# Kernel tuning notes

Hardware: AMD Instinct MI355X
Metric: run time of the kernel (lower is better)

The kernel has to match this reference:

```python
import jax, jax.numpy as jnp
import numpy as np
import math

D_MODEL = 1024
N_HEADS = 16
D_FF = 4096
KERNEL = 25
EPS = 1e-5


def setup_inputs() -> dict:
    key = jax.random.key(0)
    ks = jax.random.split(key, 16)
    B, L, D = 2, 2048, D_MODEL
    s = 0.02
    inp = {
        'x': jax.random.normal(ks[0], (B, L, D), dtype=jnp.float32),
        'Wq': jax.random.normal(ks[1], (D, D), dtype=jnp.float32) * s,
        'bq': jnp.zeros((D,), jnp.float32),
        'Wk': jax.random.normal(ks[2], (D, D), dtype=jnp.float32) * s,
        'bk': jnp.zeros((D,), jnp.float32),
        'Wv': jax.random.normal(ks[3], (D, D), dtype=jnp.float32) * s,
        'bv': jnp.zeros((D,), jnp.float32),
        'Wo': jax.random.normal(ks[4], (D, D), dtype=jnp.float32) * s,
        'bo': jnp.zeros((D,), jnp.float32),
        'W1': jax.random.normal(ks[5], (D_FF, D), dtype=jnp.float32) * s,
        'b1': jnp.zeros((D_FF,), jnp.float32),
        'W2': jax.random.normal(ks[6], (D, D_FF), dtype=jnp.float32) * s,
        'b2': jnp.zeros((D,), jnp.float32),
        'g1': jnp.ones((D,), jnp.float32),
        'be1': jnp.zeros((D,), jnp.float32),
        'g2': jnp.ones((D,), jnp.float32),
        'be2': jnp.zeros((D,), jnp.float32),
    }
    return inp


def moving_avg(x):
    # torch AvgPool1d(kernel=25, stride=1, padding=12, count_include_pad=True)
    # x: (B, L, D) -> trend: (B, L, D)
    pad = KERNEL // 2
    xp = jnp.pad(x, ((0, 0), (pad, pad), (0, 0)))
    c = jnp.cumsum(xp, axis=1)
    c = jnp.concatenate([jnp.zeros_like(c[:, :1]), c], axis=1)
    return (c[:, KERNEL:] - c[:, :-KERNEL]) / KERNEL


def layernorm(x, g, b):
    mu = jnp.mean(x, axis=-1, keepdims=True)
    var = jnp.mean((x - mu) ** 2, axis=-1, keepdims=True)
    return (x - mu) * jax.lax.rsqrt(var + EPS) * g + b


def reference(x, Wq, bq, Wk, bk, Wv, bv, Wo, bo, W1, b1, W2, b2, g1, be1, g2, be2):
    B, L, D = x.shape
    H, dk = N_HEADS, D // N_HEADS
    # projections (torch Linear: y = x @ W.T + b)
    q = (x @ Wq.T + bq).reshape(B, L, H, dk).transpose(0, 2, 1, 3)
    k = (x @ Wk.T + bk).reshape(B, L, H, dk).transpose(0, 2, 1, 3)
    v = (x @ Wv.T + bv).reshape(B, L, H, dk).transpose(0, 2, 1, 3)
    scores = jnp.einsum('bhld,bhmd->bhlm', q, k) / math.sqrt(dk)
    t = jnp.arange(L, dtype=jnp.float32)
    time_bias = -0.1 * jnp.abs(t[None, :] - t[:, None])  # (L, L)
    attn = jax.nn.softmax(scores + time_bias[None, None], axis=-1)
    ao = jnp.einsum('bhlm,bhmd->bhld', attn, v)
    ao = ao.transpose(0, 2, 1, 3).reshape(B, L, D)
    attn_out = ao @ Wo.T + bo
    x = x + attn_out
    x = moving_avg(x)  # trend kept (x, _ = decomp1(x))
    x = layernorm(x, g1, be1)
    ff = jax.nn.gelu(x @ W1.T + b1, approximate=False) @ W2.T + b2
    x = x + ff
    x = moving_avg(x)  # trend kept again
    x = layernorm(x, g2, be2)
    return x
```

## Files before the change

kernel.cpp:

```cpp
#include <hip/hip_runtime.h>
#include <hip/hip_bf16.h>
#include <math.h>

#define DMODEL 1024
#define LSEQ   2048
#define BATCH  2
#define NHEADS 16
#define DHEAD  64
#define DFF    4096
#define MROWS  (BATCH*LSEQ)

typedef __attribute__((ext_vector_type(8))) short short8;
typedef __attribute__((ext_vector_type(4))) float f32x4;
using bf16 = __hip_bfloat16;

static __device__ __forceinline__ f32x4 mfma16(short8 a, short8 b, f32x4 c) {
    return __builtin_amdgcn_mfma_f32_16x16x32_bf16(a, b, c, 0, 0, 0);
}

static __device__ __forceinline__ void gload16(const void* g, void* l) {
    __builtin_amdgcn_global_load_lds(
        (const __attribute__((address_space(1))) char*)g,
        (__attribute__((address_space(3))) char*)l, 16, 0, 0);
}

static __device__ __forceinline__ bf16 b16(float v) { return __float2bfloat16(v); }

__global__ void f2b1_kernel(const float* __restrict__ in, bf16* __restrict__ out, int n4) {
    int i = blockIdx.x * blockDim.x + threadIdx.x;
    if (i >= n4) return;
    float4 v = reinterpret_cast<const float4*>(in)[i];
    union { ushort4 u; bf16 h[4]; } o;
    o.h[0] = b16(v.x); o.h[1] = b16(v.y); o.h[2] = b16(v.z); o.h[3] = b16(v.w);
    reinterpret_cast<ushort4*>(out)[i] = o.u;
}

__global__ void f2b4_kernel(const float* p0, const float* p1, const float* p2, const float* p3,
                            bf16* o0, bf16* o1, bf16* o2, bf16* o3, int n4) {
    const float* in; bf16* out;
    switch (blockIdx.y) {
        case 0: in = p0; out = o0; break;
        case 1: in = p1; out = o1; break;
        case 2: in = p2; out = o2; break;
        default: in = p3; out = o3; break;
    }
    int i = blockIdx.x * blockDim.x + threadIdx.x;
    if (i >= n4) return;
    float4 v = reinterpret_cast<const float4*>(in)[i];
    union { ushort4 u; bf16 h[4]; } o;
    o.h[0] = b16(v.x); o.h[1] = b16(v.y); o.h[2] = b16(v.z); o.h[3] = b16(v.w);
    reinterpret_cast<ushort4*>(out)[i] = o.u;
}

__global__ void concat3_kernel(const float* __restrict__ a, const float* __restrict__ b,
                               const float* __restrict__ c, float* __restrict__ o) {
    int i = blockIdx.x * blockDim.x + threadIdx.x;
    if (i < DMODEL) { o[i] = a[i]; o[DMODEL + i] = b[i]; o[2 * DMODEL + i] = c[i]; }
}

template<int S>
__global__ __launch_bounds__(256) void reduce_kernel(const float* __restrict__ res,
                                                     const float* __restrict__ P,
                                                     const float* __restrict__ bias,
                                                     float* __restrict__ out, int n4) {
    int i = blockIdx.x * blockDim.x + threadIdx.x;
    if (i >= n4) return;
    float4 acc = reinterpret_cast<const float4*>(res)[i];
#pragma unroll
    for (int s = 0; s < S; ++s) {
        float4 p = reinterpret_cast<const float4*>(P)[i + (size_t)s * (MROWS * DMODEL / 4)];
        acc.x += p.x; acc.y += p.y; acc.z += p.z; acc.w += p.w;
    }
    float4 bs = reinterpret_cast<const float4*>(bias)[i & (DMODEL / 4 - 1)];
    acc.x += bs.x; acc.y += bs.y; acc.z += bs.z; acc.w += bs.w;
    reinterpret_cast<float4*>(out)[i] = acc;
}

template<int EPI>
__global__ __launch_bounds__(512, 2) void gemm256(const bf16* __restrict__ A,
                                                  const bf16* __restrict__ W,
                                                  const float* __restrict__ bias,
                                                  void* __restrict__ Cout,
                                                  int M, int N, int lda, int ldw,
                                                  int K, int nn) {
    __shared__ bf16 sm[49152];
    const int t    = threadIdx.x;
    const int wave = t >> 6, lane = t & 63;
    const int lr   = lane & 15, lkb = lane >> 4;
    const int wm   = wave >> 2, wn = wave & 3;
    const int sk   = blockIdx.z;

    const int nwg = gridDim.x;
    const int bid = blockIdx.x;
    const int wg  = (bid & 7) * (nwg >> 3) + (bid >> 3);
    const int m0  = (wg / nn) * 256;
    const int n0  = (wg % nn) * 256;

    const bf16* src[4];
    int dbase[4];
#pragma unroll
    for (int u = 0; u < 4; ++u) {
        const int q  = t + (u & 1) * 512;
        const int R  = q >> 3;
        const int ss = (q & 7) ^ (R & 7);
        const int rp = ss >> 2, c = (ss & 3) * 8;
        if (u < 2) src[u] = A + (size_t)(m0 + 2 * R + rp) * lda + (size_t)sk * K + c;
        else       src[u] = W + (size_t)(n0 + 2 * R + rp) * ldw + (size_t)sk * K + c;
        dbase[u] = ((u >> 1) ? 16384 : 0) + (wave * 64 + (u & 1) * 512) * 16;
    }
    char* smb = (char*)sm;

    int aoff[8], boff[4];
#pragma unroll
    for (int i = 0; i < 8; ++i) {
        const int r = wm * 128 + i * 16 + lr, R = r >> 1;
        aoff[i] = R * 128 + ((((r & 1) << 2) | lkb) ^ (R & 7)) * 16;
    }
#pragma unroll
    for (int j = 0; j < 4; ++j) {
        const int r = wn * 64 + j * 16 + lr, R = r >> 1;
        boff[j] = 16384 + R * 128 + ((((r & 1) << 2) | lkb) ^ (R & 7)) * 16;
    }

    f32x4 acc[8][4];
#pragma unroll
    for (int i = 0; i < 8; ++i)
#pragma unroll
        for (int j = 0; j < 4; ++j)
            acc[i][j] = (f32x4){0.f, 0.f, 0.f, 0.f};

    const int nt = K >> 5;
    auto STAGE = [&](int bufoff, int kt) {
        const int koff = kt * 32;
#pragma unroll
        for (int u = 0; u < 4; ++u)
            gload16(src[u] + koff, smb + bufoff + dbase[u]);
    };

    STAGE(0, 0);
    if (nt > 1) STAGE(32768, 1);
    __builtin_amdgcn_sched_barrier(0);
    if (nt > 1) asm volatile("s_waitcnt vmcnt(4)" ::: "memory");
    else        asm volatile("s_waitcnt vmcnt(0)" ::: "memory");
    __builtin_amdgcn_s_barrier();
    __builtin_amdgcn_sched_barrier(0);

    int curoff = 0, stgoff = 65536;
    for (int kt = 0; kt < nt; ++kt) {
        if (kt + 2 < nt) {
            STAGE(stgoff, kt + 2);
            stgoff = (stgoff == 65536) ? 0 : stgoff + 32768;
        }
        short8 a[8], b[4];
#pragma unroll
        for (int i = 0; i < 8; ++i)
            a[i] = *reinterpret_cast<const short8*>(smb + curoff + aoff[i]);
#pragma unroll
        for (int j = 0; j < 4; ++j)
            b[j] = *reinterpret_cast<const short8*>(smb + curoff + boff[j]);
#pragma unroll
        for (int i = 0; i < 8; ++i)
#pragma unroll
            for (int j = 0; j < 4; ++j)
                acc[i][j] = mfma16(b[j], a[i], acc[i][j]);
        if (kt + 1 < nt) {
            __builtin_amdgcn_sched_barrier(0);
            if (kt + 2 < nt) asm volatile("s_waitcnt vmcnt(4)" ::: "memory");
            else             asm volatile("s_waitcnt vmcnt(0)" ::: "memory");
            __builtin_amdgcn_s_barrier();
            __builtin_amdgcn_sched_barrier(0);
        }
        curoff = (curoff == 65536) ? 0 : curoff + 32768;
    }

    float* Cp = (float*)Cout + (EPI == 3 ? (size_t)sk * M * N : 0);
#pragma unroll
    for (int i = 0; i < 8; ++i) {
        const int row = m0 + wm * 128 + i * 16 + lr;
#pragma unroll
        for (int j = 0; j < 4; ++j) {
            const int col = n0 + wn * 64 + j * 16 + lkb * 4;
            f32x4 v = acc[i][j];
            if (EPI != 3) {
                float4 bs = *reinterpret_cast<const float4*>(&bias[col]);
                v[0] += bs.x; v[1] += bs.y; v[2] += bs.z; v[3] += bs.w;
            }
            if (EPI == 0 || EPI == 3) {
                float4 ov; ov.x = v[0]; ov.y = v[1]; ov.z = v[2]; ov.w = v[3];
                *reinterpret_cast<float4*>(&Cp[(size_t)row * N + col]) = ov;
            } else if (EPI == 1) {
                union { ushort4 u; bf16 h[4]; } ob;
#pragma unroll
                for (int q = 0; q < 4; ++q) {
                    float x = v[q];
                    float u2 = x * (1.5957691216f + 0.0713548162f * x * x);
                    float e = __expf(fminf(u2, 60.f));
                    ob.h[q] = b16(x * (e / (e + 1.f)));
                }
                *reinterpret_cast<ushort4*>(
                    &reinterpret_cast<bf16*>(Cout)[(size_t)row * N + col]) = ob.u;
            } else {
                union { ushort4 u; bf16 h[4]; } ob;
#pragma unroll
                for (int q = 0; q < 4; ++q) ob.h[q] = b16(v[q]);
                *reinterpret_cast<ushort4*>(
                    &reinterpret_cast<bf16*>(Cout)[(size_t)row * N + col]) = ob.u;
            }
        }
    }
}

__global__ __launch_bounds__(256) void attn_kernel(const bf16* __restrict__ Q,
                                                   const bf16* __restrict__ Km,
                                                   const bf16* __restrict__ V,
                                                   bf16* __restrict__ O,
                                                   int ldq, int ldo) {
    __shared__ bf16 Qs[64][72];
    __shared__ bf16 Ks[64][72];
    __shared__ bf16 VsT[64][72];
    __shared__ bf16 Ps[64][72];
    const int t    = threadIdx.x;
    const int wave = t >> 6, lane = t & 63;
    const int lr   = lane & 15, lkb = lane >> 4;
    const int qt   = blockIdx.x;
    const int q0   = qt * 64;
    const int b    = blockIdx.y >> 4, h = blockIdx.y & 15;
    const size_t base  = (size_t)b * LSEQ * ldq + (size_t)h * DHEAD;
    const size_t baseo = (size_t)b * LSEQ * ldo + (size_t)h * DHEAD;

#pragma unroll
    for (int p = 0; p < 2; ++p) {
        int idx = t + p * 256;
        int row = idx >> 3, c = (idx & 7) * 8;
        *reinterpret_cast<uint4*>(&Qs[row][c]) =
            *reinterpret_cast<const uint4*>(&Q[base + (size_t)(q0 + row) * ldq + c]);
    }
    __syncthreads();
    short8 qa[2];
    qa[0] = *reinterpret_cast<const short8*>(&Qs[wave * 16 + lr][lkb * 8]);
    qa[1] = *reinterpret_cast<const short8*>(&Qs[wave * 16 + lr][32 + lkb * 8]);

    f32x4 o[4];
#pragma unroll
    for (int dj = 0; dj < 4; ++dj) o[dj] = (f32x4){0.f, 0.f, 0.f, 0.f};
    float mrun[4], lrun[4];
#pragma unroll
    for (int q = 0; q < 4; ++q) { mrun[q] = -1e30f; lrun[q] = 0.f; }

    int kt0 = qt - 3; if (kt0 < 0) kt0 = 0;
    int kt1 = qt + 3; if (kt1 > LSEQ / 64 - 1) kt1 = LSEQ / 64 - 1;

    for (int kt = kt0; kt <= kt1; ++kt) {
        const int k0 = kt * 64;
        __syncthreads();
#pragma unroll
        for (int p = 0; p < 2; ++p) {
            int idx = t + p * 256;
            int row = idx >> 3, c = (idx & 7) * 8;
            *reinterpret_cast<uint4*>(&Ks[row][c]) =
                *reinterpret_cast<const uint4*>(&Km[base + (size_t)(k0 + row) * ldq + c]);
        }
        {
            const int vl = lane, vw = wave;
#pragma unroll
            for (int p = 0; p < 2; ++p) {
                int c = vw * 8 + p * 32;
                union { uint4 u; bf16 hh[8]; } tv;
                tv.u = *reinterpret_cast<const uint4*>(&V[base + (size_t)(k0 + vl) * ldq + c]);
#pragma unroll
                for (int e = 0; e < 8; ++e) VsT[c + e][vl] = tv.hh[e];
            }
        }
        __syncthreads();

        f32x4 s[4];
#pragma unroll
        for (int j = 0; j < 4; ++j) {
            short8 kb0 = *reinterpret_cast<const short8*>(&Ks[j * 16 + lr][lkb * 8]);
            short8 kb1 = *reinterpret_cast<const short8*>(&Ks[j * 16 + lr][32 + lkb * 8]);
            f32x4 z = (f32x4){0.f, 0.f, 0.f, 0.f};
            z = mfma16(qa[0], kb0, z);
            z = mfma16(qa[1], kb1, z);
            s[j] = z;
        }
        float mx[4];
#pragma unroll
        for (int q = 0; q < 4; ++q) mx[q] = -1e30f;
#pragma unroll
        for (int j = 0; j < 4; ++j) {
            int cm = k0 + j * 16 + lr;
#pragma unroll
            for (int q = 0; q < 4; ++q) {
                int rq = q0 + wave * 16 + lkb * 4 + q;
                float sv = s[j][q] * 0.125f - 0.1f * fabsf((float)(rq - cm));
                s[j][q] = sv;
                mx[q] = fmaxf(mx[q], sv);
            }
        }
#pragma unroll
        for (int q = 0; q < 4; ++q) {
#pragma unroll
            for (int off = 1; off < 16; off <<= 1)
                mx[q] = fmaxf(mx[q], __shfl_xor(mx[q], off));
        }
        float alpha[4];
#pragma unroll
        for (int q = 0; q < 4; ++q) {
            float mnew = fmaxf(mrun[q], mx[q]);
            alpha[q] = __expf(mrun[q] - mnew);
            mrun[q] = mnew;
        }
        float rs[4] = {0.f, 0.f, 0.f, 0.f};
#pragma unroll
        for (int j = 0; j < 4; ++j) {
#pragma unroll
            for (int q = 0; q < 4; ++q) {
                float p = __expf(s[j][q] - mrun[q]);
                rs[q] += p;
                Ps[wave * 16 + lkb * 4 + q][j * 16 + lr] = b16(p);
            }
        }
#pragma unroll
        for (int q = 0; q < 4; ++q) {
#pragma unroll
            for (int off = 1; off < 16; off <<= 1)
                rs[q] += __shfl_xor(rs[q], off);
            lrun[q] = lrun[q] * alpha[q] + rs[q];
        }
#pragma unroll
        for (int dj = 0; dj < 4; ++dj)
#pragma unroll
            for (int q = 0; q < 4; ++q) o[dj][q] *= alpha[q];

        short8 pa0 = *reinterpret_cast<const short8*>(&Ps[wave * 16 + lr][lkb * 8]);
        short8 pa1 = *reinterpret_cast<const short8*>(&Ps[wave * 16 + lr][32 + lkb * 8]);
#pragma unroll
        for (int dj = 0; dj < 4; ++dj) {
            short8 vb0 = *reinterpret_cast<const short8*>(&VsT[dj * 16 + lr][lkb * 8]);
            short8 vb1 = *reinterpret_cast<const short8*>(&VsT[dj * 16 + lr][32 + lkb * 8]);
            o[dj] = mfma16(pa0, vb0, o[dj]);
            o[dj] = mfma16(pa1, vb1, o[dj]);
        }
    }

#pragma unroll
    for (int dj = 0; dj < 4; ++dj) {
#pragma unroll
        for (int q = 0; q < 4; ++q) {
            int row = q0 + wave * 16 + lkb * 4 + q;
            int col = dj * 16 + lr;
            float val = o[dj][q] / lrun[q];
            O[baseo + (size_t)row * ldo + col] = b16(val);
        }
    }
}

__global__ __launch_bounds__(256) void mavg_ln_kernel(const float* __restrict__ r,
                                                      const float* __restrict__ g,
                                                      const float* __restrict__ be,
                                                      float* __restrict__ out,
                                                      bf16* __restrict__ outb) {
    const int row = (blockIdx.x & 7) * (MROWS / 8) + (blockIdx.x >> 3);
    const int b = row >> 11, l = row & 2047;
    const int t = threadIdx.x, c = t * 4;
    const float* base = r + (size_t)b * LSEQ * DMODEL;
    int j0 = l - 12; if (j0 < 0) j0 = 0;
    int j1 = l + 12; if (j1 > LSEQ - 1) j1 = LSEQ - 1;
    float s0 = 0.f, s1 = 0.f, s2 = 0.f, s3 = 0.f;
    for (int j = j0; j <= j1; ++j) {
        float4 v = *reinterpret_cast<const float4*>(&base[(size_t)j * DMODEL + c]);
        s0 += v.x; s1 += v.y; s2 += v.z; s3 += v.w;
    }
    const float kinv = 1.0f / 25.0f;
    float t0 = s0 * kinv, t1 = s1 * kinv, t2 = s2 * kinv, t3 = s3 * kinv;
    float p1 = t0 + t1 + t2 + t3;
    float p2 = t0 * t0 + t1 * t1 + t2 * t2 + t3 * t3;
    const int lane = t & 63, wv = t >> 6;
#pragma unroll
    for (int off = 1; off < 64; off <<= 1) {
        p1 += __shfl_xor(p1, off);
        p2 += __shfl_xor(p2, off);
    }
    __shared__ float red[8];
    if (lane == 0) { red[wv] = p1; red[4 + wv] = p2; }
    __syncthreads();
    p1 = red[0] + red[1] + red[2] + red[3];
    p2 = red[4] + red[5] + red[6] + red[7];
    const float mu  = p1 * (1.0f / 1024.0f);
    const float var = p2 * (1.0f / 1024.0f) - mu * mu;
    const float inv = rsqrtf(var + 1e-5f);
    float4 gg = *reinterpret_cast<const float4*>(&g[c]);
    float4 bb = *reinterpret_cast<const float4*>(&be[c]);
    float o0 = (t0 - mu) * inv * gg.x + bb.x;
    float o1 = (t1 - mu) * inv * gg.y + bb.y;
    float o2 = (t2 - mu) * inv * gg.z + bb.z;
    float o3 = (t3 - mu) * inv * gg.w + bb.w;
    float4 ov; ov.x = o0; ov.y = o1; ov.z = o2; ov.w = o3;
    *reinterpret_cast<float4*>(&out[(size_t)row * DMODEL + c]) = ov;
    if (outb) {
        union { ushort4 u; bf16 hh[4]; } ob;
        ob.hh[0] = b16(o0); ob.hh[1] = b16(o1); ob.hh[2] = b16(o2); ob.hh[3] = b16(o3);
        reinterpret_cast<ushort4*>(outb + (size_t)row * DMODEL)[t] = ob.u;
    }
}

extern "C" void kernel_launch(void* const* d_in, const int* in_sizes, int n_in,
                              void* d_out, int out_size, void* d_ws, size_t ws_size,
                              hipStream_t stream) {
    const float* x   = (const float*)d_in[0];
    const float* Wq  = (const float*)d_in[1];
    const float* bq  = (const float*)d_in[2];
    const float* Wk  = (const float*)d_in[3];
    const float* bk  = (const float*)d_in[4];
    const float* Wv  = (const float*)d_in[5];
    const float* bv  = (const float*)d_in[6];
    const float* Wo  = (const float*)d_in[7];
    const float* bo  = (const float*)d_in[8];
    const float* W1  = (const float*)d_in[9];
    const float* b1  = (const float*)d_in[10];
    const float* W2  = (const float*)d_in[11];
    const float* b2  = (const float*)d_in[12];
    const float* g1  = (const float*)d_in[13];
    const float* be1 = (const float*)d_in[14];
    const float* g2  = (const float*)d_in[15];
    const float* be2 = (const float*)d_in[16];
    float* out = (float*)d_out;
    char* ws = (char*)d_ws;
    const size_t MB = 1u << 20;

    float* rr   = (float*)(ws + 0);
    bf16* xb    = (bf16*)(ws + 0);
    bf16* qkvb  = (bf16*)(ws + 16 * MB);
    bf16* ab    = (bf16*)(ws + 16 * MB);
    bf16* hb    = (bf16*)(ws + 24 * MB);
    bf16* aob   = (bf16*)(ws + 40 * MB);
    bf16* Wqkvb = (bf16*)(ws + 48 * MB);
    bf16* Wob   = (bf16*)(ws + 54 * MB);
    bf16* W1b   = (bf16*)(ws + 56 * MB);
    bf16* W2b   = (bf16*)(ws + 64 * MB);
    float* P    = (float*)(ws + 72 * MB);
    float* a    = (float*)(ws + 136 * MB);
    float* bqkv = (float*)(ws + 136 * MB);

    f2b1_kernel<<<(MROWS * DMODEL / 4) / 256, 256, 0, stream>>>(x, xb, MROWS * DMODEL / 4);
    f2b4_kernel<<<dim3((DMODEL * DMODEL / 4) / 256, 4), 256, 0, stream>>>(
        Wq, Wk, Wv, Wo,
        Wqkvb, Wqkvb + DMODEL * DMODEL, Wqkvb + 2 * DMODEL * DMODEL, Wob,
        DMODEL * DMODEL / 4);
    f2b4_kernel<<<dim3((DFF * DMODEL / 4) / 256, 2), 256, 0, stream>>>(
        W1, W2, nullptr, nullptr, W1b, W2b, nullptr, nullptr, DFF * DMODEL / 4);
    concat3_kernel<<<4, 256, 0, stream>>>(bq, bk, bv, bqkv);

    gemm256<2><<<dim3(192, 1, 1), 512, 0, stream>>>(xb, Wqkvb, bqkv, qkvb,
                                                    MROWS, 3 * DMODEL, DMODEL, DMODEL, DMODEL, 12);
    attn_kernel<<<dim3(32, 32), 256, 0, stream>>>(qkvb, qkvb + DMODEL, qkvb + 2 * DMODEL,
                                                  aob, 3 * DMODEL, DMODEL);
    gemm256<3><<<dim3(64, 1, 4), 512, 0, stream>>>(aob, Wob, nullptr, P,
                                                   MROWS, DMODEL, DMODEL, DMODEL, DMODEL / 4, 4);
    reduce_kernel<4><<<(MROWS * DMODEL / 4) / 256, 256, 0, stream>>>(x, P, bo, rr, MROWS * DMODEL / 4);
    mavg_ln_kernel<<<MROWS, 256, 0, stream>>>(rr, g1, be1, a, ab);
    gemm256<1><<<dim3(256, 1, 1), 512, 0, stream>>>(ab, W1b, b1, hb,
                                                    MROWS, DFF, DMODEL, DMODEL, DMODEL, 16);
    gemm256<3><<<dim3(64, 1, 4), 512, 0, stream>>>(hb, W2b, nullptr, P,
                                                   MROWS, DMODEL, DFF, DFF, DFF / 4, 4);
    reduce_kernel<4><<<(MROWS * DMODEL / 4) / 256, 256, 0, stream>>>(a, P, b2, rr, MROWS * DMODEL / 4);
    mavg_ln_kernel<<<MROWS, 256, 0, stream>>>(rr, g2, be2, out, nullptr);
}
```

Measured before the change: 285.8 us.

## Use 128x128 GEMM tiles, bf16 two-way split-K partials, narrower attention window

Replaces the 256x256, 512-thread GEMM with a 128x128, 256-thread variant that allows 3 blocks per CU and launches more workgroups. It also raises wave priority around the MFMA block. Split-K for the Wo and W2 GEMMs drops from 4 to 2, and the partial sums are stored in bf16 rather than fp32, which cuts partial-buffer traffic in both the GEMMs and the reduce kernel. The attention key-tile window shrinks from ±3 to ±2 tiles, relying on the time-bias decay to skip more work. In exchange, accuracy drops from the bf16 partials and from the truncated attention band, and the smaller tiles give less data reuse per block.

```diff
diff --git a/kernel.cpp b/kernel.cpp
--- a/kernel.cpp
+++ b/kernel.cpp
@@ -60,7 +60,7 @@
 
 template<int S>
 __global__ __launch_bounds__(256) void reduce_kernel(const float* __restrict__ res,
-                                                     const float* __restrict__ P,
+                                                     const bf16* __restrict__ P,
                                                      const float* __restrict__ bias,
                                                      float* __restrict__ out, int n4) {
     int i = blockIdx.x * blockDim.x + threadIdx.x;
@@ -68,8 +68,12 @@
     float4 acc = reinterpret_cast<const float4*>(res)[i];
 #pragma unroll
     for (int s = 0; s < S; ++s) {
-        float4 p = reinterpret_cast<const float4*>(P)[i + (size_t)s * (MROWS * DMODEL / 4)];
-        acc.x += p.x; acc.y += p.y; acc.z += p.z; acc.w += p.w;
+        union { ushort4 u; bf16 h[4]; } p;
+        p.u = reinterpret_cast<const ushort4*>(P)[i + (size_t)s * (MROWS * DMODEL / 4)];
+        acc.x += __bfloat162float(p.h[0]);
+        acc.y += __bfloat162float(p.h[1]);
+        acc.z += __bfloat162float(p.h[2]);
+        acc.w += __bfloat162float(p.h[3]);
     }
     float4 bs = reinterpret_cast<const float4*>(bias)[i & (DMODEL / 4 - 1)];
     acc.x += bs.x; acc.y += bs.y; acc.z += bs.z; acc.w += bs.w;
@@ -77,54 +81,55 @@
 }
 
 template<int EPI>
-__global__ __launch_bounds__(512, 2) void gemm256(const bf16* __restrict__ A,
+__global__ __launch_bounds__(256, 3) void gemm128(const bf16* __restrict__ A,
                                                   const bf16* __restrict__ W,
                                                   const float* __restrict__ bias,
                                                   void* __restrict__ Cout,
                                                   int M, int N, int lda, int ldw,
                                                   int K, int nn) {
-    __shared__ bf16 sm[49152];
+    __shared__ bf16 sm[24576];
     const int t    = threadIdx.x;
     const int wave = t >> 6, lane = t & 63;
     const int lr   = lane & 15, lkb = lane >> 4;
-    const int wm   = wave >> 2, wn = wave & 3;
+    const int wr   = (wave >> 1) * 64;
+    const int wc   = (wave & 1) * 64;
     const int sk   = blockIdx.z;
 
     const int nwg = gridDim.x;
     const int bid = blockIdx.x;
     const int wg  = (bid & 7) * (nwg >> 3) + (bid >> 3);
-    const int m0  = (wg / nn) * 256;
-    const int n0  = (wg % nn) * 256;
+    const int m0  = (wg / nn) * 128;
+    const int n0  = (wg % nn) * 128;
 
     const bf16* src[4];
     int dbase[4];
 #pragma unroll
     for (int u = 0; u < 4; ++u) {
-        const int q  = t + (u & 1) * 512;
+        const int q  = t + (u & 1) * 256;
         const int R  = q >> 3;
         const int ss = (q & 7) ^ (R & 7);
         const int rp = ss >> 2, c = (ss & 3) * 8;
         if (u < 2) src[u] = A + (size_t)(m0 + 2 * R + rp) * lda + (size_t)sk * K + c;
         else       src[u] = W + (size_t)(n0 + 2 * R + rp) * ldw + (size_t)sk * K + c;
-        dbase[u] = ((u >> 1) ? 16384 : 0) + (wave * 64 + (u & 1) * 512) * 16;
+        dbase[u] = ((u >> 1) ? 8192 : 0) + (u & 1) * 4096 + wave * 1024;
     }
     char* smb = (char*)sm;
 
-    int aoff[8], boff[4];
-#pragma unroll
-    for (int i = 0; i < 8; ++i) {
-        const int r = wm * 128 + i * 16 + lr, R = r >> 1;
+    int aoff[4], boff[4];
+#pragma unroll
+    for (int i = 0; i < 4; ++i) {
+        const int r = wr + i * 16 + lr, R = r >> 1;
         aoff[i] = R * 128 + ((((r & 1) << 2) | lkb) ^ (R & 7)) * 16;
     }
 #pragma unroll
     for (int j = 0; j < 4; ++j) {
-        const int r = wn * 64 + j * 16 + lr, R = r >> 1;
-        boff[j] = 16384 + R * 128 + ((((r & 1) << 2) | lkb) ^ (R & 7)) * 16;
-    }
-
-    f32x4 acc[8][4];
-#pragma unroll
-    for (int i = 0; i < 8; ++i)
+        const int r = wc + j * 16 + lr, R = r >> 1;
+        boff[j] = 8192 + R * 128 + ((((r & 1) << 2) | lkb) ^ (R & 7)) * 16;
+    }
+
+    f32x4 acc[4][4];
+#pragma unroll
+    for (int i = 0; i < 4; ++i)
 #pragma unroll
         for (int j = 0; j < 4; ++j)
             acc[i][j] = (f32x4){0.f, 0.f, 0.f, 0.f};
@@ -138,56 +143,56 @@
     };
 
     STAGE(0, 0);
-    if (nt > 1) STAGE(32768, 1);
+    if (nt > 1) STAGE(16384, 1);
     __builtin_amdgcn_sched_barrier(0);
     if (nt > 1) asm volatile("s_waitcnt vmcnt(4)" ::: "memory");
     else        asm volatile("s_waitcnt vmcnt(0)" ::: "memory");
     __builtin_amdgcn_s_barrier();
     __builtin_amdgcn_sched_barrier(0);
 
-    int curoff = 0, stgoff = 65536;
+    int curoff = 0, stgoff = 32768;
     for (int kt = 0; kt < nt; ++kt) {
-        if (kt + 2 < nt) {
-            STAGE(stgoff, kt + 2);
-            stgoff = (stgoff == 65536) ? 0 : stgoff + 32768;
-        }
-        short8 a[8], b[4];
-#pragma unroll
-        for (int i = 0; i < 8; ++i)
+        const bool pre = (kt + 2 < nt);
+        if (pre) STAGE(stgoff, kt + 2);
+        short8 a[4], b[4];
+#pragma unroll
+        for (int i = 0; i < 4; ++i)
             a[i] = *reinterpret_cast<const short8*>(smb + curoff + aoff[i]);
 #pragma unroll
         for (int j = 0; j < 4; ++j)
             b[j] = *reinterpret_cast<const short8*>(smb + curoff + boff[j]);
-#pragma unroll
-        for (int i = 0; i < 8; ++i)
+        __builtin_amdgcn_s_setprio(1);
+#pragma unroll
+        for (int i = 0; i < 4; ++i)
 #pragma unroll
             for (int j = 0; j < 4; ++j)
                 acc[i][j] = mfma16(b[j], a[i], acc[i][j]);
+        __builtin_amdgcn_s_setprio(0);
         if (kt + 1 < nt) {
             __builtin_amdgcn_sched_barrier(0);
-            if (kt + 2 < nt) asm volatile("s_waitcnt vmcnt(4)" ::: "memory");
-            else             asm volatile("s_waitcnt vmcnt(0)" ::: "memory");
+            if (pre) asm volatile("s_waitcnt vmcnt(4)" ::: "memory");
+            else     asm volatile("s_waitcnt vmcnt(0)" ::: "memory");
             __builtin_amdgcn_s_barrier();
             __builtin_amdgcn_sched_barrier(0);
         }
-        curoff = (curoff == 65536) ? 0 : curoff + 32768;
-    }
-
-    float* Cp = (float*)Cout + (EPI == 3 ? (size_t)sk * M * N : 0);
-#pragma unroll
-    for (int i = 0; i < 8; ++i) {
-        const int row = m0 + wm * 128 + i * 16 + lr;
+        if (pre) stgoff = (stgoff == 32768) ? 0 : stgoff + 16384;
+        curoff = (curoff == 32768) ? 0 : curoff + 16384;
+    }
+
+#pragma unroll
+    for (int i = 0; i < 4; ++i) {
+        const int row = m0 + wr + i * 16 + lr;
 #pragma unroll
         for (int j = 0; j < 4; ++j) {
-            const int col = n0 + wn * 64 + j * 16 + lkb * 4;
+            const int col = n0 + wc + j * 16 + lkb * 4;
             f32x4 v = acc[i][j];
             if (EPI != 3) {
                 float4 bs = *reinterpret_cast<const float4*>(&bias[col]);
                 v[0] += bs.x; v[1] += bs.y; v[2] += bs.z; v[3] += bs.w;
             }
-            if (EPI == 0 || EPI == 3) {
+            if (EPI == 0) {
                 float4 ov; ov.x = v[0]; ov.y = v[1]; ov.z = v[2]; ov.w = v[3];
-                *reinterpret_cast<float4*>(&Cp[(size_t)row * N + col]) = ov;
+                *reinterpret_cast<float4*>(&((float*)Cout)[(size_t)row * N + col]) = ov;
             } else if (EPI == 1) {
                 union { ushort4 u; bf16 h[4]; } ob;
 #pragma unroll
@@ -199,12 +204,18 @@
                 }
                 *reinterpret_cast<ushort4*>(
                     &reinterpret_cast<bf16*>(Cout)[(size_t)row * N + col]) = ob.u;
-            } else {
+            } else if (EPI == 2) {
                 union { ushort4 u; bf16 h[4]; } ob;
 #pragma unroll
                 for (int q = 0; q < 4; ++q) ob.h[q] = b16(v[q]);
                 *reinterpret_cast<ushort4*>(
                     &reinterpret_cast<bf16*>(Cout)[(size_t)row * N + col]) = ob.u;
+            } else {
+                bf16* Pp = (bf16*)Cout + (size_t)sk * M * N;
+                union { ushort4 u; bf16 h[4]; } ob;
+#pragma unroll
+                for (int q = 0; q < 4; ++q) ob.h[q] = b16(v[q]);
+                *reinterpret_cast<ushort4*>(&Pp[(size_t)row * N + col]) = ob.u;
             }
         }
     }
@@ -247,8 +258,8 @@
 #pragma unroll
     for (int q = 0; q < 4; ++q) { mrun[q] = -1e30f; lrun[q] = 0.f; }
 
-    int kt0 = qt - 3; if (kt0 < 0) kt0 = 0;
-    int kt1 = qt + 3; if (kt1 > LSEQ / 64 - 1) kt1 = LSEQ / 64 - 1;
+    int kt0 = qt - 2; if (kt0 < 0) kt0 = 0;
+    int kt1 = qt + 2; if (kt1 > LSEQ / 64 - 1) kt1 = LSEQ / 64 - 1;
 
     for (int kt = kt0; kt <= kt1; ++kt) {
         const int k0 = kt * 64;
@@ -438,7 +449,7 @@
     bf16* Wob   = (bf16*)(ws + 54 * MB);
     bf16* W1b   = (bf16*)(ws + 56 * MB);
     bf16* W2b   = (bf16*)(ws + 64 * MB);
-    float* P    = (float*)(ws + 72 * MB);
+    bf16* P     = (bf16*)(ws + 72 * MB);
     float* a    = (float*)(ws + 136 * MB);
     float* bqkv = (float*)(ws + 136 * MB);
 
@@ -451,18 +462,18 @@
         W1, W2, nullptr, nullptr, W1b, W2b, nullptr, nullptr, DFF * DMODEL / 4);
     concat3_kernel<<<4, 256, 0, stream>>>(bq, bk, bv, bqkv);
 
-    gemm256<2><<<dim3(192, 1, 1), 512, 0, stream>>>(xb, Wqkvb, bqkv, qkvb,
-                                                    MROWS, 3 * DMODEL, DMODEL, DMODEL, DMODEL, 12);
+    gemm128<2><<<dim3(768, 1, 1), 256, 0, stream>>>(xb, Wqkvb, bqkv, qkvb,
+                                                    MROWS, 3 * DMODEL, DMODEL, DMODEL, DMODEL, 24);
     attn_kernel<<<dim3(32, 32), 256, 0, stream>>>(qkvb, qkvb + DMODEL, qkvb + 2 * DMODEL,
                                                   aob, 3 * DMODEL, DMODEL);
-    gemm256<3><<<dim3(64, 1, 4), 512, 0, stream>>>(aob, Wob, nullptr, P,
-                                                   MROWS, DMODEL, DMODEL, DMODEL, DMODEL / 4, 4);
-    reduce_kernel<4><<<(MROWS * DMODEL / 4) / 256, 256, 0, stream>>>(x, P, bo, rr, MROWS * DMODEL / 4);
+    gemm128<3><<<dim3(256, 1, 2), 256, 0, stream>>>(aob, Wob, nullptr, P,
+                                                    MROWS, DMODEL, DMODEL, DMODEL, DMODEL / 2, 8);
+    reduce_kernel<2><<<(MROWS * DMODEL / 4) / 256, 256, 0, stream>>>(x, P, bo, rr, MROWS * DMODEL / 4);
     mavg_ln_kernel<<<MROWS, 256, 0, stream>>>(rr, g1, be1, a, ab);
-    gemm256<1><<<dim3(256, 1, 1), 512, 0, stream>>>(ab, W1b, b1, hb,
-                                                    MROWS, DFF, DMODEL, DMODEL, DMODEL, 16);
-    gemm256<3><<<dim3(64, 1, 4), 512, 0, stream>>>(hb, W2b, nullptr, P,
-                                                   MROWS, DMODEL, DFF, DFF, DFF / 4, 4);
-    reduce_kernel<4><<<(MROWS * DMODEL / 4) / 256, 256, 0, stream>>>(a, P, b2, rr, MROWS * DMODEL / 4);
+    gemm128<1><<<dim3(1024, 1, 1), 256, 0, stream>>>(ab, W1b, b1, hb,
+                                                     MROWS, DFF, DMODEL, DMODEL, DMODEL, 32);
+    gemm128<3><<<dim3(256, 1, 2), 256, 0, stream>>>(hb, W2b, nullptr, P,
+                                                    MROWS, DMODEL, DFF, DFF, DFF / 2, 8);
+    reduce_kernel<2><<<(MROWS * DMODEL / 4) / 256, 256, 0, stream>>>(a, P, b2, rr, MROWS * DMODEL / 4);
     mavg_ln_kernel<<<MROWS, 256, 0, stream>>>(rr, g2, be2, out, nullptr);
 }
```

Result: faster. 266.4 us (-6.8%).
